# Optimization experiments

Measured on AMD Instinct MI355X. Metric: run time of the kernel, lower is better.

Reference implementation:

```python
import jax, jax.numpy as jnp
import numpy as np

B, T, D1, D2, DM, V, K = 2, 512, 256, 128, 1024, 32000, 4
SCALE = 0.05  # keep tanh/sigmoid out of full saturation with randn params


def setup_inputs() -> dict:
    key = jax.random.key(0)
    ks = jax.random.split(key, 7)
    s = lambda k, shape: SCALE * jax.random.normal(k, shape, dtype=jnp.float32)
    return {
        "gc": jax.random.normal(ks[0], (B, T, D1), dtype=jnp.float32),
        "H": s(ks[1], (K, DM, D1)),
        "U": s(ks[2], (K, D2, D1)),
        "v": s(ks[3], (V, D2)),
        "u": s(ks[4], (K, D1)),
        "b": s(ks[5], (V, K)),
        "emb": s(ks[6], (V, DM)),
    }


def reference(gc, H, U, v, u, b, emb):
    # gc: (B,T,D1)
    hc = jnp.tanh(jnp.einsum('kdi,bti->btkd', H, gc))        # (B,T,K,DM)
    tU = jnp.tanh(jnp.einsum('kji,bti->btkj', U, gc))        # (B,T,K,D2)
    # token- and context-dependent gate logits: (B,T,V,K)
    lc = (jnp.einsum('vj,btkj->btvk', v, tU)
          + jnp.einsum('ki,bti->btk', u, gc)[:, :, None, :]
          + b[None, None])
    gamma = jax.nn.sigmoid(lc[..., :K - 1])                  # (B,T,V,3)
    g0, g1, g2 = gamma[..., 0], gamma[..., 1], gamma[..., 2]
    # sigmoid-tree mixture priors: (B,T,V,K)
    pi = jnp.stack([g0 * g1, g0 * (1.0 - g1),
                    (1.0 - g0) * g2, (1.0 - g0) * (1.0 - g2)], axis=-1)
    # contract hc with embeddings per gate FIRST (avoids btikj blow-up),
    # then weight by pi -- same math as the original pi (x) emb outer product.
    dots = jnp.einsum('btkd,vd->btvk', hc, emb)              # (B,T,V,K)
    logits = jnp.sum(pi * dots, axis=-1)                     # (B,T,V)
    return jax.nn.softmax(logits, axis=-1)
```

## Files before the change

### kernel.cpp

```cpp
#include <hip/hip_runtime.h>
#include <math.h>

namespace {

typedef _Float16 f16;
typedef _Float16 f16x8 __attribute__((ext_vector_type(8)));
typedef float    f32x4 __attribute__((ext_vector_type(4)));

constexpr int kBT = 1024, kD1 = 256, kD2 = 128, kDM = 1024, kV = 32000, kK = 4;
constexpr int AR = kBT * kK;
constexpr int ROWS_H = kK * kDM;
constexpr int ROWS_U = kK * kD2;
constexpr int ROWS_ALL = ROWS_H + ROWS_U + kK;
constexpr int HALF_ROWS = ROWS_ALL / 2;

__global__ __launch_bounds__(256) void prep_gemm(
    const float* __restrict__ gc, const float* __restrict__ Hm,
    const float* __restrict__ Um, const float* __restrict__ um,
    f16* __restrict__ hc, f16* __restrict__ tu, float* __restrict__ ug)
{
    __shared__ float sgc[8][kD1];
    const int btBase = blockIdx.x * 8;
    for (int idx = threadIdx.x; idx < 8 * kD1; idx += 256)
        sgc[idx / kD1][idx % kD1] = gc[(size_t)btBase * kD1 + idx];
    __syncthreads();

    const int rStart = blockIdx.y * HALF_ROWS;
    const int rEnd   = rStart + HALF_ROWS;
    for (int r = rStart + (int)threadIdx.x; r < rEnd; r += 256) {
        const float* wrow;
        if (r < ROWS_H)               wrow = Hm + (size_t)r * kD1;
        else if (r < ROWS_H + ROWS_U) wrow = Um + (size_t)(r - ROWS_H) * kD1;
        else                          wrow = um + (size_t)(r - ROWS_H - ROWS_U) * kD1;

        float acc[8] = {0.f,0.f,0.f,0.f,0.f,0.f,0.f,0.f};
        for (int i = 0; i < kD1; i += 4) {
            const float4 w = *reinterpret_cast<const float4*>(wrow + i);
            #pragma unroll
            for (int b = 0; b < 8; ++b) {
                const float4 g = *reinterpret_cast<const float4*>(&sgc[b][i]);
                acc[b] = fmaf(w.x, g.x, acc[b]);
                acc[b] = fmaf(w.y, g.y, acc[b]);
                acc[b] = fmaf(w.z, g.z, acc[b]);
                acc[b] = fmaf(w.w, g.w, acc[b]);
            }
        }
        #pragma unroll
        for (int b = 0; b < 8; ++b) {
            const int bt = btBase + b;
            if (r < ROWS_H) {
                const int k = r >> 10, d = r & 1023;
                hc[((size_t)(bt * kK + k) << 10) + d] = (f16)tanhf(acc[b]);
            } else if (r < ROWS_H + ROWS_U) {
                const int r2 = r - ROWS_H;
                const int k = r2 >> 7, j = r2 & 127;
                tu[(size_t)(bt * kK + k) * kD2 + j] = (f16)tanhf(acc[b]);
            } else {
                ug[bt * kK + (r - ROWS_H - ROWS_U)] = acc[b];
            }
        }
    }
}

__global__ __launch_bounds__(256) void cvt_kernel(
    const float* __restrict__ src, f16* __restrict__ dst, int n8)
{
    const int i = blockIdx.x * 256 + threadIdx.x;
    if (i >= n8) return;
    const float4 x0 = *reinterpret_cast<const float4*>(src + (size_t)i * 8);
    const float4 x1 = *reinterpret_cast<const float4*>(src + (size_t)i * 8 + 4);
    union { f16 h[8]; uint4 v; } u;
    u.h[0] = (f16)x0.x; u.h[1] = (f16)x0.y; u.h[2] = (f16)x0.z; u.h[3] = (f16)x0.w;
    u.h[4] = (f16)x1.x; u.h[5] = (f16)x1.y; u.h[6] = (f16)x1.z; u.h[7] = (f16)x1.w;
    *reinterpret_cast<uint4*>(dst + (size_t)i * 8) = u.v;
}

__device__ __forceinline__ uint packf16x2(float a, float b) {
    union { f16 h[2]; uint u; } z;
    z.h[0] = (f16)a; z.h[1] = (f16)b;
    return z.u;
}

__global__ __launch_bounds__(512, 2) void fused_mfma(
    const f16* __restrict__ hc,  const f16* __restrict__ tu,
    const f16* __restrict__ v16, const f16* __restrict__ e16,
    const float* __restrict__ ug, const float* __restrict__ bmat,
    float* __restrict__ out)
{
    __shared__ __align__(16) f16 sA[4][256 * 32];
    __shared__ __align__(16) f16 sB[4][128 * 32];

    const int tid  = threadIdx.x;
    const int lane = tid & 63;
    const int wave = tid >> 6;
    const int fr = lane & 15, fq = lane >> 4;
    const int wm = wave >> 1, wc = wave & 1;

    const int wg  = blockIdx.x;
    const int idx = wg >> 3;
    const int bx  = (wg & 7) * 2 + idx / 250;
    const int by  = idx % 250;
    const int aRowBase = bx * 256;
    const int vBase    = by * 128;

    const int srowL = lane >> 2;
    const int scolL = (lane & 3) * 8;

    auto stage_any = [&](int g, bool gate) {
        const f16* A = gate ? tu : hc;
        const f16* B = gate ? v16 : e16;
        const int stride = gate ? kD2 : kDM;
        const int colb = (gate ? g : (g - 4)) * 32 + scolL;
        const int slot = g & 3;
        #pragma unroll
        for (int i = 0; i < 2; ++i) {
            const int c = wave * 2 + i;
            const f16* src = A + (size_t)(aRowBase + c * 16 + srowL) * stride + colb;
            __builtin_amdgcn_global_load_lds(
                (const __attribute__((address_space(1))) void*)src,
                (__attribute__((address_space(3))) void*)(&sA[slot][c * 512]), 16, 0, 0);
        }
        const f16* srcb = B + (size_t)(vBase + wave * 16 + srowL) * stride + colb;
        __builtin_amdgcn_global_load_lds(
            (const __attribute__((address_space(1))) void*)srcb,
            (__attribute__((address_space(3))) void*)(&sB[slot][wave * 512]), 16, 0, 0);
    };
    auto stage = [&](int g) { stage_any(g, g < 4); };
    auto stage_d = [&](int g) { stage_any(g, false); };

#define PHASE(G, ACC, DO_STAGE, STG_FN, VM)                                   \
    {                                                                         \
        const int slot_ = (G) & 3;                                            \
        const f16* __restrict__ pa_ = &sA[slot_][0];                          \
        const f16* __restrict__ pb_ = &sB[slot_][0];                          \
        f16x8 a_[4], b_[4];                                                   \
        _Pragma("unroll")                                                     \
        for (int m = 0; m < 4; ++m)                                           \
            a_[m] = *reinterpret_cast<const f16x8*>(                          \
                pa_ + (wm * 64 + m * 16 + fr) * 32 + fq * 8);                 \
        _Pragma("unroll")                                                     \
        for (int n = 0; n < 4; ++n)                                           \
            b_[n] = *reinterpret_cast<const f16x8*>(                          \
                pb_ + (wc * 64 + n * 16 + fr) * 32 + fq * 8);                 \
        if (DO_STAGE) STG_FN((G) + 3);                                        \
        asm volatile("s_waitcnt vmcnt(" VM ")" ::: "memory");                 \
        __builtin_amdgcn_s_barrier();                                         \
        asm volatile("" ::: "memory");                                        \
        __builtin_amdgcn_s_setprio(1);                                        \
        _Pragma("unroll")                                                     \
        for (int m = 0; m < 4; ++m)                                           \
            _Pragma("unroll")                                                 \
            for (int n = 0; n < 4; ++n)                                       \
                ACC[m][n] = __builtin_amdgcn_mfma_f32_16x16x32_f16(           \
                    a_[m], b_[n], ACC[m][n], 0, 0, 0);                        \
        __builtin_amdgcn_s_setprio(0);                                        \
        asm volatile("" ::: "memory");                                        \
        __builtin_amdgcn_s_barrier();                                         \
        asm volatile("" ::: "memory");                                        \
    }

    f32x4 acc[4][4];
    const f32x4 zz = {0.f, 0.f, 0.f, 0.f};
    #pragma unroll
    for (int m = 0; m < 4; ++m)
        #pragma unroll
        for (int n = 0; n < 4; ++n) acc[m][n] = zz;

    stage(0); stage(1); stage(2);
    asm volatile("s_waitcnt vmcnt(6)" ::: "memory");
    __builtin_amdgcn_s_barrier();
    asm volatile("" ::: "memory");

    PHASE(0, acc, true, stage, "6");
    PHASE(1, acc, true, stage, "6");
    PHASE(2, acc, true, stage, "6");
    PHASE(3, acc, true, stage, "6");

    uint pi01[4][4], pi23[4][4];
    {
        const int btB = bx * 64 + wm * 16;
        float4 bb[4];
        #pragma unroll
        for (int n = 0; n < 4; ++n) {
            const int v = vBase + wc * 64 + n * 16 + fr;
            bb[n] = *reinterpret_cast<const float4*>(bmat + (size_t)v * 4);
        }
        #pragma unroll
        for (int m = 0; m < 4; ++m) {
            const float4 ugv = *reinterpret_cast<const float4*>(ug + (btB + m * 4 + fq) * 4);
            #pragma unroll
            for (int n = 0; n < 4; ++n) {
                const float l0 = acc[m][n][0] + ugv.x + bb[n].x;
                const float l1 = acc[m][n][1] + ugv.y + bb[n].y;
                const float l2 = acc[m][n][2] + ugv.z + bb[n].z;
                const float g0 = 1.f / (1.f + __expf(-l0));
                const float g1 = 1.f / (1.f + __expf(-l1));
                const float g2 = 1.f / (1.f + __expf(-l2));
                pi01[m][n] = packf16x2(g0 * g1, g0 * (1.f - g1));
                pi23[m][n] = packf16x2((1.f - g0) * g2, (1.f - g0) * (1.f - g2));
            }
        }
    }
    #pragma unroll
    for (int m = 0; m < 4; ++m)
        #pragma unroll
        for (int n = 0; n < 4; ++n) acc[m][n] = zz;

    for (int gg = 4; gg < 32; gg += 4) {
        PHASE(gg + 0, acc, true, stage_d, "6");
        PHASE(gg + 1, acc, true, stage_d, "6");
        PHASE(gg + 2, acc, true, stage_d, "6");
        PHASE(gg + 3, acc, true, stage_d, "6");
    }
    PHASE(32, acc, true,  stage_d, "6");
    PHASE(33, acc, false, stage_d, "3");
    PHASE(34, acc, false, stage_d, "0");
    PHASE(35, acc, false, stage_d, "0");
#undef PHASE

    const int btB = bx * 64 + wm * 16;
    #pragma unroll
    for (int m = 0; m < 4; ++m) {
        const int bt = btB + m * 4 + fq;
        #pragma unroll
        for (int n = 0; n < 4; ++n) {
            const int v = vBase + wc * 64 + n * 16 + fr;
            union { uint u; f16 h[2]; } p01, p23;
            p01.u = pi01[m][n]; p23.u = pi23[m][n];
            const float lg = (float)p01.h[0] * acc[m][n][0]
                           + (float)p01.h[1] * acc[m][n][1]
                           + (float)p23.h[0] * acc[m][n][2]
                           + (float)p23.h[1] * acc[m][n][3];
            out[(size_t)bt * kV + v] = lg;
        }
    }
}

__global__ __launch_bounds__(256) void softmax_kernel(float* __restrict__ out)
{
    __shared__ float red[4];
    float* row = out + (size_t)blockIdx.x * kV;
    const int tid = threadIdx.x;

    float s = 0.f;
    for (int i = tid * 4; i < kV; i += 1024) {
        const float4 x = *reinterpret_cast<const float4*>(row + i);
        s += __expf(x.x) + __expf(x.y) + __expf(x.z) + __expf(x.w);
    }
    #pragma unroll
    for (int o = 1; o < 64; o <<= 1) s += __shfl_xor(s, o);
    if ((tid & 63) == 0) red[tid >> 6] = s;
    __syncthreads();
    s = red[0] + red[1] + red[2] + red[3];
    const float inv = 1.f / s;

    for (int i = tid * 4; i < kV; i += 1024) {
        const float4 x = *reinterpret_cast<const float4*>(row + i);
        float4 y;
        y.x = __expf(x.x) * inv;
        y.y = __expf(x.y) * inv;
        y.z = __expf(x.z) * inv;
        y.w = __expf(x.w) * inv;
        *reinterpret_cast<float4*>(row + i) = y;
    }
}

}

extern "C" void kernel_launch(void* const* d_in, const int* in_sizes, int n_in,
                              void* d_out, int out_size, void* d_ws, size_t ws_size,
                              hipStream_t stream)
{
    (void)in_sizes; (void)n_in; (void)out_size; (void)ws_size;
    const float* gc   = (const float*)d_in[0];
    const float* Hm   = (const float*)d_in[1];
    const float* Um   = (const float*)d_in[2];
    const float* vmat = (const float*)d_in[3];
    const float* um   = (const float*)d_in[4];
    const float* bmat = (const float*)d_in[5];
    const float* emb  = (const float*)d_in[6];
    float* out = (float*)d_out;

    size_t off = 0;
    auto take = [&](size_t bytes) -> char* {
        char* p = (char*)d_ws + off;
        off += (bytes + 255) & ~(size_t)255;
        return p;
    };
    f16*   hc  = (f16*)  take((size_t)AR * kDM * 2);
    f16*   tu  = (f16*)  take((size_t)AR * kD2 * 2);
    f16*   v16 = (f16*)  take((size_t)kV * kD2 * 2);
    f16*   e16 = (f16*)  take((size_t)kV * kDM * 2);
    float* ug  = (float*)take((size_t)AR * 4);

    prep_gemm<<<dim3(kBT / 8, 2), 256, 0, stream>>>(gc, Hm, Um, um, hc, tu, ug);
    cvt_kernel<<<(kV * kD2 / 8 + 255) / 256, 256, 0, stream>>>(vmat, v16, kV * kD2 / 8);
    cvt_kernel<<<(kV * kDM / 8 + 255) / 256, 256, 0, stream>>>(emb, e16, kV * kDM / 8);
    fused_mfma<<<dim3((AR / 256) * (kV / 128)), 512, 0, stream>>>(
        hc, tu, v16, e16, ug, bmat, out);
    softmax_kernel<<<dim3(kBT), 256, 0, stream>>>(out);
}
```

Measured before the change: 631.3 us.

## Fuse softmax partial sums into GEMM epilogue, swizzle LDS, simplify grid mapping

The GEMM epilogue now computes per-tile exp sums and writes them to a partial-sum buffer, so the softmax kernel no longer makes a full read-and-exp pass over the logits to get the denominator. The LDS layout is XOR-swizzled on both the global-to-LDS stores and the fragment reads to reduce bank conflicts. The bias and ug loads are hoisted ahead of the last gate phases to hide their latency. The 1D grid with a remapped block order is replaced by a plain 2D grid, which changes L2 reuse patterns.

```diff
diff --git a/kernel.cpp b/kernel.cpp
--- a/kernel.cpp
+++ b/kernel.cpp
@@ -13,6 +13,7 @@
 constexpr int ROWS_U = kK * kD2;
 constexpr int ROWS_ALL = ROWS_H + ROWS_U + kK;
 constexpr int HALF_ROWS = ROWS_ALL / 2;
+constexpr int NBY = kV / 128;
 
 __global__ __launch_bounds__(256) void prep_gemm(
     const float* __restrict__ gc, const float* __restrict__ Hm,
@@ -85,7 +86,7 @@
     const f16* __restrict__ hc,  const f16* __restrict__ tu,
     const f16* __restrict__ v16, const f16* __restrict__ e16,
     const float* __restrict__ ug, const float* __restrict__ bmat,
-    float* __restrict__ out)
+    float* __restrict__ out, float* __restrict__ psum)
 {
     __shared__ __align__(16) f16 sA[4][256 * 32];
     __shared__ __align__(16) f16 sB[4][128 * 32];
@@ -96,15 +97,16 @@
     const int fr = lane & 15, fq = lane >> 4;
     const int wm = wave >> 1, wc = wave & 1;
 
-    const int wg  = blockIdx.x;
-    const int idx = wg >> 3;
-    const int bx  = (wg & 7) * 2 + idx / 250;
-    const int by  = idx % 250;
+    const int bx = blockIdx.x;
+    const int by = blockIdx.y;
     const int aRowBase = bx * 256;
     const int vBase    = by * 128;
+    const int btB      = bx * 64 + wm * 16;
 
     const int srowL = lane >> 2;
-    const int scolL = (lane & 3) * 8;
+    const int scolL = ((lane & 3) ^ ((lane >> 3) & 3)) * 8;
+
+    const int rslot = (fq ^ ((fr >> 1) & 3)) * 8;
 
     auto stage_any = [&](int g, bool gate) {
         const f16* A = gate ? tu : hc;
@@ -137,11 +139,11 @@
         _Pragma("unroll")                                                     \
         for (int m = 0; m < 4; ++m)                                           \
             a_[m] = *reinterpret_cast<const f16x8*>(                          \
-                pa_ + (wm * 64 + m * 16 + fr) * 32 + fq * 8);                 \
+                pa_ + (wm * 64 + m * 16 + fr) * 32 + rslot);                  \
         _Pragma("unroll")                                                     \
         for (int n = 0; n < 4; ++n)                                           \
             b_[n] = *reinterpret_cast<const f16x8*>(                          \
-                pb_ + (wc * 64 + n * 16 + fr) * 32 + fq * 8);                 \
+                pb_ + (wc * 64 + n * 16 + fr) * 32 + rslot);                  \
         if (DO_STAGE) STG_FN((G) + 3);                                        \
         asm volatile("s_waitcnt vmcnt(" VM ")" ::: "memory");                 \
         __builtin_amdgcn_s_barrier();                                         \
@@ -173,32 +175,32 @@
 
     PHASE(0, acc, true, stage, "6");
     PHASE(1, acc, true, stage, "6");
+
+    float4 bb[4], ugv[4];
+    #pragma unroll
+    for (int n = 0; n < 4; ++n)
+        bb[n] = *reinterpret_cast<const float4*>(
+            bmat + (size_t)(vBase + wc * 64 + n * 16 + fr) * 4);
+    #pragma unroll
+    for (int m = 0; m < 4; ++m)
+        ugv[m] = *reinterpret_cast<const float4*>(ug + (btB + m * 4 + fq) * 4);
+
     PHASE(2, acc, true, stage, "6");
     PHASE(3, acc, true, stage, "6");
 
     uint pi01[4][4], pi23[4][4];
-    {
-        const int btB = bx * 64 + wm * 16;
-        float4 bb[4];
+    #pragma unroll
+    for (int m = 0; m < 4; ++m) {
         #pragma unroll
         for (int n = 0; n < 4; ++n) {
-            const int v = vBase + wc * 64 + n * 16 + fr;
-            bb[n] = *reinterpret_cast<const float4*>(bmat + (size_t)v * 4);
-        }
-        #pragma unroll
-        for (int m = 0; m < 4; ++m) {
-            const float4 ugv = *reinterpret_cast<const float4*>(ug + (btB + m * 4 + fq) * 4);
-            #pragma unroll
-            for (int n = 0; n < 4; ++n) {
-                const float l0 = acc[m][n][0] + ugv.x + bb[n].x;
-                const float l1 = acc[m][n][1] + ugv.y + bb[n].y;
-                const float l2 = acc[m][n][2] + ugv.z + bb[n].z;
-                const float g0 = 1.f / (1.f + __expf(-l0));
-                const float g1 = 1.f / (1.f + __expf(-l1));
-                const float g2 = 1.f / (1.f + __expf(-l2));
-                pi01[m][n] = packf16x2(g0 * g1, g0 * (1.f - g1));
-                pi23[m][n] = packf16x2((1.f - g0) * g2, (1.f - g0) * (1.f - g2));
-            }
+            const float l0 = acc[m][n][0] + ugv[m].x + bb[n].x;
+            const float l1 = acc[m][n][1] + ugv[m].y + bb[n].y;
+            const float l2 = acc[m][n][2] + ugv[m].z + bb[n].z;
+            const float g0 = 1.f / (1.f + __expf(-l0));
+            const float g1 = 1.f / (1.f + __expf(-l1));
+            const float g2 = 1.f / (1.f + __expf(-l2));
+            pi01[m][n] = packf16x2(g0 * g1, g0 * (1.f - g1));
+            pi23[m][n] = packf16x2((1.f - g0) * g2, (1.f - g0) * (1.f - g2));
         }
     }
     #pragma unroll
@@ -218,10 +220,10 @@
     PHASE(35, acc, false, stage_d, "0");
 #undef PHASE
 
-    const int btB = bx * 64 + wm * 16;
     #pragma unroll
     for (int m = 0; m < 4; ++m) {
         const int bt = btB + m * 4 + fq;
+        float es = 0.f;
         #pragma unroll
         for (int n = 0; n < 4; ++n) {
             const int v = vBase + wc * 64 + n * 16 + fr;
@@ -232,21 +234,27 @@
                            + (float)p23.h[0] * acc[m][n][2]
                            + (float)p23.h[1] * acc[m][n][3];
             out[(size_t)bt * kV + v] = lg;
-        }
-    }
-}
-
-__global__ __launch_bounds__(256) void softmax_kernel(float* __restrict__ out)
+            es += __expf(lg);
+        }
+        es += __shfl_xor(es, 1);
+        es += __shfl_xor(es, 2);
+        es += __shfl_xor(es, 4);
+        es += __shfl_xor(es, 8);
+        if (fr == 0)
+            psum[(size_t)bt * 512 + by * 2 + wc] = es;
+    }
+}
+
+__global__ __launch_bounds__(256) void softmax_kernel(
+    float* __restrict__ out, const float* __restrict__ psum)
 {
     __shared__ float red[4];
-    float* row = out + (size_t)blockIdx.x * kV;
+    const int bt = blockIdx.x;
+    float* row = out + (size_t)bt * kV;
     const int tid = threadIdx.x;
 
     float s = 0.f;
-    for (int i = tid * 4; i < kV; i += 1024) {
-        const float4 x = *reinterpret_cast<const float4*>(row + i);
-        s += __expf(x.x) + __expf(x.y) + __expf(x.z) + __expf(x.w);
-    }
+    for (int i = tid; i < 2 * NBY; i += 256) s += psum[(size_t)bt * 512 + i];
     #pragma unroll
     for (int o = 1; o < 64; o <<= 1) s += __shfl_xor(s, o);
     if ((tid & 63) == 0) red[tid >> 6] = s;
@@ -287,16 +295,17 @@
         off += (bytes + 255) & ~(size_t)255;
         return p;
     };
-    f16*   hc  = (f16*)  take((size_t)AR * kDM * 2);
-    f16*   tu  = (f16*)  take((size_t)AR * kD2 * 2);
-    f16*   v16 = (f16*)  take((size_t)kV * kD2 * 2);
-    f16*   e16 = (f16*)  take((size_t)kV * kDM * 2);
-    float* ug  = (float*)take((size_t)AR * 4);
+    f16*   hc   = (f16*)  take((size_t)AR * kDM * 2);
+    f16*   tu   = (f16*)  take((size_t)AR * kD2 * 2);
+    f16*   v16  = (f16*)  take((size_t)kV * kD2 * 2);
+    f16*   e16  = (f16*)  take((size_t)kV * kDM * 2);
+    float* ug   = (float*)take((size_t)AR * 4);
+    float* psum = (float*)take((size_t)kBT * 512 * 4);
 
     prep_gemm<<<dim3(kBT / 8, 2), 256, 0, stream>>>(gc, Hm, Um, um, hc, tu, ug);
     cvt_kernel<<<(kV * kD2 / 8 + 255) / 256, 256, 0, stream>>>(vmat, v16, kV * kD2 / 8);
     cvt_kernel<<<(kV * kDM / 8 + 255) / 256, 256, 0, stream>>>(emb, e16, kV * kDM / 8);
-    fused_mfma<<<dim3((AR / 256) * (kV / 128)), 512, 0, stream>>>(
-        hc, tu, v16, e16, ug, bmat, out);
-    softmax_kernel<<<dim3(kBT), 256, 0, stream>>>(out);
-}
+    fused_mfma<<<dim3(AR / 256, NBY), 512, 0, stream>>>(
+        hc, tu, v16, e16, ug, bmat, out, psum);
+    softmax_kernel<<<dim3(kBT), 256, 0, stream>>>(out, psum);
+}
```

Result: faster. 600.4 us (-4.9%).
